# Performance work log

Measured on AMD Instinct MI355X. Metric: run time of the kernel, lower is better.

## Reference

```python
import math
import jax, jax.numpy as jnp
import numpy as np

B, P = 256, 256


def setup_inputs() -> dict:
    key = jax.random.key(0)
    ks = jax.random.split(key, 12)
    sc = 1.0 / math.sqrt(P)
    A = jax.random.normal(ks[0], (B, P, P), jnp.float32) * 0.01
    Theta = jnp.eye(P, dtype=jnp.float32) + 0.5 * (A + A.transpose(0, 2, 1))
    Wb = jax.random.normal(ks[1], (B, P, P), jnp.float32) * 0.01
    W_init = jnp.eye(P, dtype=jnp.float32) + 0.5 * (Wb + Wb.transpose(0, 2, 1))
    return {
        "Theta": Theta,
        "W_init": W_init,
        "Wc": jax.random.normal(ks[2], (P - 1, P - 1), jnp.float32) * sc,
        "bc": jax.random.normal(ks[3], (P - 1,), jnp.float32) * 0.01,
        "A1": jax.random.normal(ks[4], (P, P), jnp.float32) * sc,
        "b1": jax.random.normal(ks[5], (P,), jnp.float32) * 0.01,
        "A2": jax.random.normal(ks[6], (P, P), jnp.float32) * sc,
        "b2": jax.random.normal(ks[7], (P,), jnp.float32) * 0.01,
        "A3": jax.random.normal(ks[8], (1, P), jnp.float32) * sc,
        "b3": jax.random.normal(ks[9], (1,), jnp.float32) * 0.01,
    }


def _spodnet_forward(Theta, W, Wc, bc, A1, b1, A2, b2, A3, b3):
    p = Theta.shape[-1]
    scale = 1.0 / math.sqrt(p)
    # minus_idx[col] = arange(p) with `col` removed  -> [p, p-1]
    minus_idx = jnp.asarray(
        np.array([[j for j in range(p) if j != c] for c in range(p)], dtype=np.int32)
    )

    # ---- pass 1: sequential off-diagonal column update via col_learner ----
    def pass1(Th, col):
        idx = minus_idx[col]                       # [p-1]
        th12 = Th[:, idx, col]                     # [B, p-1]
        th12n = (th12 @ Wc.T + bc) * scale         # Linear(p-1,p-1)/sqrt(p)
        Th = Th.at[:, idx, col].set(th12n)
        Th = Th.at[:, col, idx].set(th12n)
        return Th, None

    Theta, _ = jax.lax.scan(pass1, Theta, jnp.arange(p))

    # ---- pass 2: sequential diagonal + Sherman-Morrison W update ----
    def pass2(carry, col):
        Th, W = carry
        idx = minus_idx[col]
        th12 = Th[:, idx, col]                     # [B, p-1]
        th22 = Th[:, col, col]                     # [B]
        W11 = W[:, idx[:, None], idx[None, :]]     # [B, p-1, p-1]
        w22 = W[:, col, col]                       # [B]
        w12 = W[:, idx, col]                       # [B, p-1]
        # inv(Theta_11) = W_11 - w_12 w_12^T / w_22
        invT11 = W11 - (w12[:, :, None] * w12[:, None, :]) / w22[:, None, None]
        v = jnp.einsum('bij,bj->bi', invT11, th12)          # [B, p-1]
        schur = jnp.einsum('bi,bi->b', th12, v)             # theta_12^T invT11 theta_12
        feats = jnp.concatenate([th22[:, None], th12], -1)  # [B, p]
        h = jax.nn.relu(feats @ A1.T + b1)
        h = jax.nn.relu(h @ A2.T + b2)
        gy = jnp.exp(h @ A3.T + b3)[:, 0]                   # [B], positive
        Th = Th.at[:, col, col].set(gy + schur)
        w22n = 1.0 / gy
        w12n = -w22n[:, None] * v
        W11n = invT11 + gy[:, None, None] * (w12n[:, :, None] * w12n[:, None, :])
        W = W.at[:, idx[:, None], idx[None, :]].set(W11n)
        W = W.at[:, idx, col].set(w12n)
        W = W.at[:, col, idx].set(w12n)
        W = W.at[:, col, col].set(w22n)
        # original detaches every W write -> no grad flows through W history
        W = jax.lax.stop_gradient(W)
        return (Th, W), None

    (Theta, _W), _ = jax.lax.scan(
        pass2, (Theta, jax.lax.stop_gradient(W)), jnp.arange(p)
    )
    return Theta


def reference(Theta, W_init, Wc, bc, A1, b1, A2, b2, A3, b3):
    # K = 1 pass (init_kwargs K=1)
    return _spodnet_forward(Theta, W_init, Wc, bc, A1, b1, A2, b2, A3, b3)
```

## Files before the change

kernel.cpp:

```cpp
#include <hip/hip_runtime.h>
#include <math.h>

#define P    256
#define PM1  255

__global__ void __launch_bounds__(256) k_transpose(
    const float* __restrict__ A1, const float* __restrict__ A2,
    float* __restrict__ A1T, float* __restrict__ A2T) {
  __shared__ float tile[64][65];
  const int bid = blockIdx.x;
  const float* src = (bid < 16) ? A1 : A2;
  float* dst       = (bid < 16) ? A1T : A2T;
  const int tl = bid & 15;
  const int R0 = (tl >> 2) << 6;
  const int C0 = (tl & 3) << 6;
  const int tx = threadIdx.x & 63;
  const int ty = threadIdx.x >> 6;
#pragma unroll
  for (int k = 0; k < 16; k++) {
    const int r = (k << 2) + ty;
    tile[r][tx] = src[(R0 + r) * P + C0 + tx];
  }
  __syncthreads();
#pragma unroll
  for (int k = 0; k < 16; k++) {
    const int c = (k << 2) + ty;
    dst[(C0 + c) * P + R0 + tx] = tile[tx][c];
  }
}

__global__ void __launch_bounds__(512, 2) k_pass1(
    float* __restrict__ Th,
    const float* __restrict__ Wc,
    const float* __restrict__ bc) {
  const int b    = blockIdx.x;
  const int tid  = threadIdx.x;
  const int lane = tid & 63;
  const int wid  = tid >> 6;
  const int wrr  = wid >> 2;
  const int wcb  = wid & 3;
  const int r0   = (wrr << 7) + lane;
  const int r1   = r0 + 64;
  const int cbase = wcb << 6;

  float w0[64], w1[64];
#pragma unroll
  for (int k = 0; k < 64; k++) {
    const int c = cbase + k;
    w0[k] = (r0 < PM1 && c < PM1) ? Wc[r0 * PM1 + c] : 0.f;
    w1[k] = (r1 < PM1 && c < PM1) ? Wc[r1 * PM1 + c] : 0.f;
  }

  __shared__ __align__(16) float t_lds[P];
  __shared__ float ypart[4][P];
  __shared__ float bc_lds[P];
  if (tid < P) bc_lds[tid] = (tid < PM1) ? bc[tid] : 0.f;

  float* __restrict__ ThB = Th + (size_t)b * P * P;
  __syncthreads();

  for (int col = 0; col < P; col++) {
    if (tid < P) {
      float v = 0.f;
      if (tid < PM1) {
        const int i = tid + (tid >= col ? 1 : 0);
        v = ThB[i * P + col];
      }
      t_lds[tid] = v;
    }
    __syncthreads();

    float acc0 = 0.f, acc1 = 0.f;
#pragma unroll
    for (int k4 = 0; k4 < 16; k4++) {
      const float4 t4 = *(const float4*)&t_lds[cbase + (k4 << 2)];
      const float tt[4] = {t4.x, t4.y, t4.z, t4.w};
#pragma unroll
      for (int kk = 0; kk < 4; kk++) {
        acc0 = fmaf(w0[(k4 << 2) + kk], tt[kk], acc0);
        acc1 = fmaf(w1[(k4 << 2) + kk], tt[kk], acc1);
      }
    }
    ypart[wcb][r0] = acc0;
    ypart[wcb][r1] = acc1;
    __syncthreads();

    if (tid < PM1) {
      const float y = (ypart[0][tid] + ypart[1][tid] + ypart[2][tid] +
                       ypart[3][tid] + bc_lds[tid]) * 0.0625f;
      const int iout = tid + (tid >= col ? 1 : 0);
      ThB[iout * P + col] = y;
      ThB[col * P + iout] = y;
    }
    __threadfence_block();
    __syncthreads();
  }
}

__global__ void __launch_bounds__(256, 4) k_mlp(
    const float* __restrict__ Th,
    const float* __restrict__ A1T, const float* __restrict__ b1,
    const float* __restrict__ A2T, const float* __restrict__ b2,
    const float* __restrict__ A3,  const float* __restrict__ b3,
    float* __restrict__ gy) {
  const int m0 = blockIdx.x << 4;
  const int b  = m0 >> 8;
  const int c0 = m0 & (P - 1);
  const int t  = threadIdx.x;

  __shared__ __align__(16) float fbuf[16][260];
  __shared__ __align__(16) float hbuf[16][260];
  __shared__ float A3_lds[P];
  if (t < P) A3_lds[t] = A3[t];

  const float* __restrict__ ThB = Th + (size_t)b * P * P;

  {
    const int cc = t & 15;
    const int dr = t >> 4;
    const int c  = c0 + cc;
#pragma unroll
    for (int ii = 0; ii < 16; ii++) {
      const int i = (ii << 4) + dr;
      const float v = ThB[i * P + c];
      const int pos = (i == c) ? 0 : (i < c ? i + 1 : i);
      fbuf[cc][pos] = v;
    }
  }
  __syncthreads();

  {
    float acc[16];
    const float bv = b1[t];
#pragma unroll
    for (int r = 0; r < 16; r++) acc[r] = bv;
    for (int j4 = 0; j4 < 64; j4++) {
      const int j = j4 << 2;
      const float a0 = A1T[(j + 0) * P + t];
      const float a1 = A1T[(j + 1) * P + t];
      const float a2 = A1T[(j + 2) * P + t];
      const float a3 = A1T[(j + 3) * P + t];
#pragma unroll
      for (int r = 0; r < 16; r++) {
        const float4 f4 = *(const float4*)&fbuf[r][j];
        acc[r] = fmaf(f4.x, a0, acc[r]);
        acc[r] = fmaf(f4.y, a1, acc[r]);
        acc[r] = fmaf(f4.z, a2, acc[r]);
        acc[r] = fmaf(f4.w, a3, acc[r]);
      }
    }
#pragma unroll
    for (int r = 0; r < 16; r++) hbuf[r][t] = fmaxf(acc[r], 0.f);
  }
  __syncthreads();

  {
    float acc[16];
    const float bv = b2[t];
#pragma unroll
    for (int r = 0; r < 16; r++) acc[r] = bv;
    for (int j4 = 0; j4 < 64; j4++) {
      const int j = j4 << 2;
      const float a0 = A2T[(j + 0) * P + t];
      const float a1 = A2T[(j + 1) * P + t];
      const float a2 = A2T[(j + 2) * P + t];
      const float a3 = A2T[(j + 3) * P + t];
#pragma unroll
      for (int r = 0; r < 16; r++) {
        const float4 f4 = *(const float4*)&hbuf[r][j];
        acc[r] = fmaf(f4.x, a0, acc[r]);
        acc[r] = fmaf(f4.y, a1, acc[r]);
        acc[r] = fmaf(f4.z, a2, acc[r]);
        acc[r] = fmaf(f4.w, a3, acc[r]);
      }
    }
    __syncthreads();
#pragma unroll
    for (int r = 0; r < 16; r++) fbuf[r][t] = fmaxf(acc[r], 0.f);
  }
  __syncthreads();

  {
    const int r = t >> 4, sub = t & 15;
    float p = 0.f;
#pragma unroll
    for (int jj = 0; jj < 16; jj++) {
      const int j = (jj << 4) + sub;
      p = fmaf(fbuf[r][j], A3_lds[j], p);
    }
    p += __shfl_xor(p, 1);
    p += __shfl_xor(p, 2);
    p += __shfl_xor(p, 4);
    p += __shfl_xor(p, 8);
    if (sub == 0) gy[m0 + r] = expf(p + b3[0]);
  }
}

__global__ void __launch_bounds__(512, 2) k_pass2(
    float* __restrict__ Th,
    const float* __restrict__ Winit,
    const float* __restrict__ gy) {
  const int b    = blockIdx.x;
  const int tid  = threadIdx.x;
  const int lane = tid & 63;
  const int wid  = tid >> 6;
  const int wrr  = wid >> 2;
  const int wcb  = wid & 3;
  const int r0   = (wrr << 7) + lane;
  const int r1   = r0 + 64;
  const int cbase = wcb << 6;

  float w0[64], w1[64];
  const float* __restrict__ WB = Winit + (size_t)b * P * P;
#pragma unroll
  for (int k4 = 0; k4 < 16; k4++) {
    const float4 v0 = *(const float4*)&WB[r0 * P + cbase + (k4 << 2)];
    const float4 v1 = *(const float4*)&WB[r1 * P + cbase + (k4 << 2)];
    w0[(k4 << 2) + 0] = v0.x; w0[(k4 << 2) + 1] = v0.y;
    w0[(k4 << 2) + 2] = v0.z; w0[(k4 << 2) + 3] = v0.w;
    w1[(k4 << 2) + 0] = v1.x; w1[(k4 << 2) + 1] = v1.y;
    w1[(k4 << 2) + 2] = v1.z; w1[(k4 << 2) + 3] = v1.w;
  }

  float* __restrict__ ThB = Th + (size_t)b * P * P;
  const float* __restrict__ gyB = gy + b * P;

  __shared__ __align__(16) float t_lds[P];
  __shared__ __align__(16) float a_lds[P];
  __shared__ __align__(16) float z_lds[P];
  __shared__ float ypart[4][P];
  __shared__ float red[8];

  float tv = 0.f;
  if (tid < P) tv = ThB[tid * P];
  __syncthreads();

  for (int col = 0; col < P; col++) {
    const int kcol  = col & 63;
    const int wccol = col >> 6;
    const float gyv = gyB[col];

    if (tid < P) t_lds[tid] = (tid == col) ? 0.f : tv;
    if (wcb == wccol) {
      float av0 = 0.f, av1 = 0.f;
#pragma unroll
      for (int k = 0; k < 64; k++) {
        if (k == kcol) { av0 = w0[k]; av1 = w1[k]; }
      }
      a_lds[r0] = av0;
      a_lds[r1] = av1;
    }
    __syncthreads();
    if (tid < P && col < PM1) tv = ThB[tid * P + col + 1];

    const float w22 = a_lds[col];
    if (tid < P) {
      float pp = a_lds[tid] * t_lds[tid];
      pp += __shfl_xor(pp, 1);  pp += __shfl_xor(pp, 2);
      pp += __shfl_xor(pp, 4);  pp += __shfl_xor(pp, 8);
      pp += __shfl_xor(pp, 16); pp += __shfl_xor(pp, 32);
      if (lane == 0) red[wid] = pp;
    }
    __syncthreads();
    const float s = (red[0] + red[1] + red[2] + red[3]) / w22;

    float acc0 = 0.f, acc1 = 0.f;
#pragma unroll
    for (int k4 = 0; k4 < 16; k4++) {
      const float4 t4 = *(const float4*)&t_lds[cbase + (k4 << 2)];
      const float tt[4] = {t4.x, t4.y, t4.z, t4.w};
#pragma unroll
      for (int kk = 0; kk < 4; kk++) {
        acc0 = fmaf(w0[(k4 << 2) + kk], tt[kk], acc0);
        acc1 = fmaf(w1[(k4 << 2) + kk], tt[kk], acc1);
      }
    }
    ypart[wcb][r0] = acc0;
    ypart[wcb][r1] = acc1;
    __syncthreads();

    if (tid < P) {
      const float y = ypart[0][tid] + ypart[1][tid] +
                      ypart[2][tid] + ypart[3][tid];
      const float v = y - a_lds[tid] * s;
      const float z = (tid == col) ? 1.f : -v;
      z_lds[tid] = z;
      float pp = t_lds[tid] * z;
      pp += __shfl_xor(pp, 1);  pp += __shfl_xor(pp, 2);
      pp += __shfl_xor(pp, 4);  pp += __shfl_xor(pp, 8);
      pp += __shfl_xor(pp, 16); pp += __shfl_xor(pp, 32);
      if (lane == 0) red[wid] = pp;
    }
    __syncthreads();
    const float schur = -(red[0] + red[1] + red[2] + red[3]);
    if (tid == 0) ThB[col * P + col] = gyv + schur;

    const float c1 = -1.f / w22;
    const float c2 = 1.f / gyv;
    const float pa0 = c1 * a_lds[r0], pa1 = c1 * a_lds[r1];
    const float pz0 = c2 * z_lds[r0], pz1 = c2 * z_lds[r1];
#pragma unroll
    for (int k4 = 0; k4 < 16; k4++) {
      const float4 a4 = *(const float4*)&a_lds[cbase + (k4 << 2)];
      const float4 z4 = *(const float4*)&z_lds[cbase + (k4 << 2)];
      const float aa[4] = {a4.x, a4.y, a4.z, a4.w};
      const float zz[4] = {z4.x, z4.y, z4.z, z4.w};
#pragma unroll
      for (int kk = 0; kk < 4; kk++) {
        const int k = (k4 << 2) + kk;
        w0[k] = fmaf(pa0, aa[kk], fmaf(pz0, zz[kk], w0[k]));
        w1[k] = fmaf(pa1, aa[kk], fmaf(pz1, zz[kk], w1[k]));
      }
    }
    __syncthreads();
  }
}

extern "C" void kernel_launch(void* const* d_in, const int* in_sizes, int n_in,
                              void* d_out, int out_size, void* d_ws, size_t ws_size,
                              hipStream_t stream) {
  (void)in_sizes; (void)n_in; (void)out_size; (void)ws_size;
  const float* Theta = (const float*)d_in[0];
  const float* Winit = (const float*)d_in[1];
  const float* Wc    = (const float*)d_in[2];
  const float* bc    = (const float*)d_in[3];
  const float* A1    = (const float*)d_in[4];
  const float* b1    = (const float*)d_in[5];
  const float* A2    = (const float*)d_in[6];
  const float* b2    = (const float*)d_in[7];
  const float* A3    = (const float*)d_in[8];
  const float* b3    = (const float*)d_in[9];
  float* out = (float*)d_out;

  float* A1T = (float*)d_ws;
  float* A2T = A1T + P * P;
  float* gy  = A2T + P * P;

  hipMemcpyAsync(out, Theta, (size_t)256 * P * P * sizeof(float),
                 hipMemcpyDeviceToDevice, stream);

  k_transpose<<<32, 256, 0, stream>>>(A1, A2, A1T, A2T);
  k_pass1<<<256, 512, 0, stream>>>(out, Wc, bc);
  k_mlp<<<4096, 256, 0, stream>>>(out, A1T, b1, A2T, b2, A3, b3, gy);
  k_pass2<<<256, 512, 0, stream>>>(out, Winit, gy);
}
```

Baseline: 1.446 ms.

## Double-buffer column vectors and cut barriers in sequential pass kernels

Both sequential column kernels now double-buffer the theta column (and W column in pass2) in LDS and prefetch the next column during the current step. This removes one or two barriers per iteration. Pass1 reads the next column row-wise, which relies on Theta staying symmetric, and forwards the freshly written value. Pass2 drops the register select-scan for the W column in favour of the owning row writing it out, and gets the Schur term from ypart in a spare wave instead of a second block reduction. The cost is more LDS, a dependence on symmetry, and more intricate ordering of reads and writes across iterations.

```diff
diff --git a/kernel.cpp b/kernel.cpp
--- a/kernel.cpp
+++ b/kernel.cpp
@@ -35,8 +35,8 @@
     const float* __restrict__ bc) {
   const int b    = blockIdx.x;
   const int tid  = threadIdx.x;
+  const int wid  = tid >> 6;
   const int lane = tid & 63;
-  const int wid  = tid >> 6;
   const int wrr  = wid >> 2;
   const int wcb  = wid & 3;
   const int r0   = (wrr << 7) + lane;
@@ -51,49 +51,51 @@
     w1[k] = (r1 < PM1 && c < PM1) ? Wc[r1 * PM1 + c] : 0.f;
   }
 
-  __shared__ __align__(16) float t_lds[P];
+  __shared__ __align__(16) float t_buf[2][P];
   __shared__ float ypart[4][P];
   __shared__ float bc_lds[P];
   if (tid < P) bc_lds[tid] = (tid < PM1) ? bc[tid] : 0.f;
 
   float* __restrict__ ThB = Th + (size_t)b * P * P;
-  __syncthreads();
-
+  if (tid < P) t_buf[0][tid] = (tid < PM1) ? ThB[tid + 1] : 0.f;
+
+  int p = 0;
   for (int col = 0; col < P; col++) {
-    if (tid < P) {
-      float v = 0.f;
-      if (tid < PM1) {
-        const int i = tid + (tid >= col ? 1 : 0);
-        v = ThB[i * P + col];
-      }
-      t_lds[tid] = v;
-    }
-    __syncthreads();
-
+    const int pn = p ^ 1;
+    __syncthreads();
     float acc0 = 0.f, acc1 = 0.f;
+    const float4* tb = (const float4*)&t_buf[p][cbase];
 #pragma unroll
     for (int k4 = 0; k4 < 16; k4++) {
-      const float4 t4 = *(const float4*)&t_lds[cbase + (k4 << 2)];
-      const float tt[4] = {t4.x, t4.y, t4.z, t4.w};
-#pragma unroll
-      for (int kk = 0; kk < 4; kk++) {
-        acc0 = fmaf(w0[(k4 << 2) + kk], tt[kk], acc0);
-        acc1 = fmaf(w1[(k4 << 2) + kk], tt[kk], acc1);
-      }
+      const float4 tv = tb[k4];
+      acc0 = fmaf(w0[(k4 << 2) + 0], tv.x, acc0);
+      acc0 = fmaf(w0[(k4 << 2) + 1], tv.y, acc0);
+      acc0 = fmaf(w0[(k4 << 2) + 2], tv.z, acc0);
+      acc0 = fmaf(w0[(k4 << 2) + 3], tv.w, acc0);
+      acc1 = fmaf(w1[(k4 << 2) + 0], tv.x, acc1);
+      acc1 = fmaf(w1[(k4 << 2) + 1], tv.y, acc1);
+      acc1 = fmaf(w1[(k4 << 2) + 2], tv.z, acc1);
+      acc1 = fmaf(w1[(k4 << 2) + 3], tv.w, acc1);
     }
     ypart[wcb][r0] = acc0;
     ypart[wcb][r1] = acc1;
-    __syncthreads();
-
+    float tnext = 0.f;
+    if (col < PM1 && tid < PM1) {
+      const int i = tid + (tid >= col + 1 ? 1 : 0);
+      tnext = ThB[(col + 1) * P + i];
+    }
+    __syncthreads();
     if (tid < PM1) {
       const float y = (ypart[0][tid] + ypart[1][tid] + ypart[2][tid] +
                        ypart[3][tid] + bc_lds[tid]) * 0.0625f;
       const int iout = tid + (tid >= col ? 1 : 0);
       ThB[iout * P + col] = y;
       ThB[col * P + iout] = y;
-    }
-    __threadfence_block();
-    __syncthreads();
+      if (col < PM1) t_buf[pn][tid] = (tid == col) ? y : tnext;
+    } else if (tid == PM1) {
+      t_buf[pn][PM1] = 0.f;
+    }
+    p = pn;
   }
 }
 
@@ -182,17 +184,17 @@
 
   {
     const int r = t >> 4, sub = t & 15;
-    float p = 0.f;
+    float pq = 0.f;
 #pragma unroll
     for (int jj = 0; jj < 16; jj++) {
       const int j = (jj << 4) + sub;
-      p = fmaf(fbuf[r][j], A3_lds[j], p);
-    }
-    p += __shfl_xor(p, 1);
-    p += __shfl_xor(p, 2);
-    p += __shfl_xor(p, 4);
-    p += __shfl_xor(p, 8);
-    if (sub == 0) gy[m0 + r] = expf(p + b3[0]);
+      pq = fmaf(fbuf[r][j], A3_lds[j], pq);
+    }
+    pq += __shfl_xor(pq, 1);
+    pq += __shfl_xor(pq, 2);
+    pq += __shfl_xor(pq, 4);
+    pq += __shfl_xor(pq, 8);
+    if (sub == 0) gy[m0 + r] = expf(pq + b3[0]);
   }
 }
 
@@ -209,6 +211,7 @@
   const int r0   = (wrr << 7) + lane;
   const int r1   = r0 + 64;
   const int cbase = wcb << 6;
+  const int e0   = lane << 2;
 
   float w0[64], w1[64];
   const float* __restrict__ WB = Winit + (size_t)b * P * P;
@@ -225,55 +228,55 @@
   float* __restrict__ ThB = Th + (size_t)b * P * P;
   const float* __restrict__ gyB = gy + b * P;
 
-  __shared__ __align__(16) float t_lds[P];
-  __shared__ __align__(16) float a_lds[P];
+  __shared__ __align__(16) float t_buf[2][P];
+  __shared__ __align__(16) float a_buf[2][P];
   __shared__ __align__(16) float z_lds[P];
   __shared__ float ypart[4][P];
-  __shared__ float red[8];
-
-  float tv = 0.f;
-  if (tid < P) tv = ThB[tid * P];
-  __syncthreads();
-
+
+  if (tid < P) t_buf[0][tid] = (tid == 0) ? 0.f : ThB[tid];
+  if (r0 == 0) {
+    float4* dst = (float4*)&a_buf[0][cbase];
+#pragma unroll
+    for (int k4 = 0; k4 < 16; k4++)
+      dst[k4] = make_float4(w0[(k4 << 2) + 0], w0[(k4 << 2) + 1],
+                            w0[(k4 << 2) + 2], w0[(k4 << 2) + 3]);
+  }
+  float gyv = gyB[0];
+
+  int p = 0;
   for (int col = 0; col < P; col++) {
-    const int kcol  = col & 63;
-    const int wccol = col >> 6;
-    const float gyv = gyB[col];
-
-    if (tid < P) t_lds[tid] = (tid == col) ? 0.f : tv;
-    if (wcb == wccol) {
-      float av0 = 0.f, av1 = 0.f;
-#pragma unroll
-      for (int k = 0; k < 64; k++) {
-        if (k == kcol) { av0 = w0[k]; av1 = w1[k]; }
-      }
-      a_lds[r0] = av0;
-      a_lds[r1] = av1;
-    }
-    __syncthreads();
-    if (tid < P && col < PM1) tv = ThB[tid * P + col + 1];
-
-    const float w22 = a_lds[col];
-    if (tid < P) {
-      float pp = a_lds[tid] * t_lds[tid];
-      pp += __shfl_xor(pp, 1);  pp += __shfl_xor(pp, 2);
-      pp += __shfl_xor(pp, 4);  pp += __shfl_xor(pp, 8);
-      pp += __shfl_xor(pp, 16); pp += __shfl_xor(pp, 32);
-      if (lane == 0) red[wid] = pp;
-    }
-    __syncthreads();
-    const float s = (red[0] + red[1] + red[2] + red[3]) / w22;
+    const int pn = p ^ 1;
+    __syncthreads();
+
+    const float4 a4 = *(const float4*)&a_buf[p][e0];
+    const float4 t4 = *(const float4*)&t_buf[p][e0];
+    float pp = a4.x * t4.x + a4.y * t4.y + a4.z * t4.z + a4.w * t4.w;
+    pp += __shfl_xor(pp, 1);  pp += __shfl_xor(pp, 2);
+    pp += __shfl_xor(pp, 4);  pp += __shfl_xor(pp, 8);
+    pp += __shfl_xor(pp, 16); pp += __shfl_xor(pp, 32);
+    const float at  = pp;
+    const float w22 = a_buf[p][col];
+    const float s   = at / w22;
+
+    float tnext = 0.f, gynext = 0.f;
+    if (col < PM1) {
+      if (tid < P) tnext = ThB[(col + 1) * P + tid];
+      gynext = gyB[col + 1];
+    }
 
     float acc0 = 0.f, acc1 = 0.f;
+    const float4* tb = (const float4*)&t_buf[p][cbase];
 #pragma unroll
     for (int k4 = 0; k4 < 16; k4++) {
-      const float4 t4 = *(const float4*)&t_lds[cbase + (k4 << 2)];
-      const float tt[4] = {t4.x, t4.y, t4.z, t4.w};
-#pragma unroll
-      for (int kk = 0; kk < 4; kk++) {
-        acc0 = fmaf(w0[(k4 << 2) + kk], tt[kk], acc0);
-        acc1 = fmaf(w1[(k4 << 2) + kk], tt[kk], acc1);
-      }
+      const float4 tv = tb[k4];
+      acc0 = fmaf(w0[(k4 << 2) + 0], tv.x, acc0);
+      acc0 = fmaf(w0[(k4 << 2) + 1], tv.y, acc0);
+      acc0 = fmaf(w0[(k4 << 2) + 2], tv.z, acc0);
+      acc0 = fmaf(w0[(k4 << 2) + 3], tv.w, acc0);
+      acc1 = fmaf(w1[(k4 << 2) + 0], tv.x, acc1);
+      acc1 = fmaf(w1[(k4 << 2) + 1], tv.y, acc1);
+      acc1 = fmaf(w1[(k4 << 2) + 2], tv.z, acc1);
+      acc1 = fmaf(w1[(k4 << 2) + 3], tv.w, acc1);
     }
     ypart[wcb][r0] = acc0;
     ypart[wcb][r1] = acc1;
@@ -282,37 +285,62 @@
     if (tid < P) {
       const float y = ypart[0][tid] + ypart[1][tid] +
                       ypart[2][tid] + ypart[3][tid];
-      const float v = y - a_lds[tid] * s;
-      const float z = (tid == col) ? 1.f : -v;
-      z_lds[tid] = z;
-      float pp = t_lds[tid] * z;
-      pp += __shfl_xor(pp, 1);  pp += __shfl_xor(pp, 2);
-      pp += __shfl_xor(pp, 4);  pp += __shfl_xor(pp, 8);
-      pp += __shfl_xor(pp, 16); pp += __shfl_xor(pp, 32);
-      if (lane == 0) red[wid] = pp;
-    }
-    __syncthreads();
-    const float schur = -(red[0] + red[1] + red[2] + red[3]);
-    if (tid == 0) ThB[col * P + col] = gyv + schur;
+      const float v = y - s * a_buf[p][tid];
+      z_lds[tid] = (tid == col) ? 1.f : -v;
+      if (col < PM1) t_buf[pn][tid] = (tid == col + 1) ? 0.f : tnext;
+    } else if (wid == 4) {
+      const float4 tt = *(const float4*)&t_buf[p][e0];
+      const float4 q0 = *(const float4*)&ypart[0][e0];
+      const float4 q1 = *(const float4*)&ypart[1][e0];
+      const float4 q2 = *(const float4*)&ypart[2][e0];
+      const float4 q3 = *(const float4*)&ypart[3][e0];
+      float sp = tt.x * (q0.x + q1.x + q2.x + q3.x)
+               + tt.y * (q0.y + q1.y + q2.y + q3.y)
+               + tt.z * (q0.z + q1.z + q2.z + q3.z)
+               + tt.w * (q0.w + q1.w + q2.w + q3.w);
+      sp += __shfl_xor(sp, 1);  sp += __shfl_xor(sp, 2);
+      sp += __shfl_xor(sp, 4);  sp += __shfl_xor(sp, 8);
+      sp += __shfl_xor(sp, 16); sp += __shfl_xor(sp, 32);
+      if (lane == 0) ThB[col * P + col] = gyv + (sp - s * at);
+    }
+    __syncthreads();
 
     const float c1 = -1.f / w22;
     const float c2 = 1.f / gyv;
-    const float pa0 = c1 * a_lds[r0], pa1 = c1 * a_lds[r1];
-    const float pz0 = c2 * z_lds[r0], pz1 = c2 * z_lds[r1];
+    const float pa0 = c1 * a_buf[p][r0], pa1 = c1 * a_buf[p][r1];
+    const float pz0 = c2 * z_lds[r0],    pz1 = c2 * z_lds[r1];
+    const float4* ab = (const float4*)&a_buf[p][cbase];
+    const float4* zb = (const float4*)&z_lds[cbase];
 #pragma unroll
     for (int k4 = 0; k4 < 16; k4++) {
-      const float4 a4 = *(const float4*)&a_lds[cbase + (k4 << 2)];
-      const float4 z4 = *(const float4*)&z_lds[cbase + (k4 << 2)];
-      const float aa[4] = {a4.x, a4.y, a4.z, a4.w};
-      const float zz[4] = {z4.x, z4.y, z4.z, z4.w};
-#pragma unroll
-      for (int kk = 0; kk < 4; kk++) {
-        const int k = (k4 << 2) + kk;
-        w0[k] = fmaf(pa0, aa[kk], fmaf(pz0, zz[kk], w0[k]));
-        w1[k] = fmaf(pa1, aa[kk], fmaf(pz1, zz[kk], w1[k]));
-      }
-    }
-    __syncthreads();
+      const float4 av = ab[k4];
+      const float4 zv = zb[k4];
+      w0[(k4 << 2) + 0] = fmaf(pa0, av.x, fmaf(pz0, zv.x, w0[(k4 << 2) + 0]));
+      w0[(k4 << 2) + 1] = fmaf(pa0, av.y, fmaf(pz0, zv.y, w0[(k4 << 2) + 1]));
+      w0[(k4 << 2) + 2] = fmaf(pa0, av.z, fmaf(pz0, zv.z, w0[(k4 << 2) + 2]));
+      w0[(k4 << 2) + 3] = fmaf(pa0, av.w, fmaf(pz0, zv.w, w0[(k4 << 2) + 3]));
+      w1[(k4 << 2) + 0] = fmaf(pa1, av.x, fmaf(pz1, zv.x, w1[(k4 << 2) + 0]));
+      w1[(k4 << 2) + 1] = fmaf(pa1, av.y, fmaf(pz1, zv.y, w1[(k4 << 2) + 1]));
+      w1[(k4 << 2) + 2] = fmaf(pa1, av.z, fmaf(pz1, zv.z, w1[(k4 << 2) + 2]));
+      w1[(k4 << 2) + 3] = fmaf(pa1, av.w, fmaf(pz1, zv.w, w1[(k4 << 2) + 3]));
+    }
+
+    if (r0 == col + 1) {
+      float4* dst = (float4*)&a_buf[pn][cbase];
+#pragma unroll
+      for (int k4 = 0; k4 < 16; k4++)
+        dst[k4] = make_float4(w0[(k4 << 2) + 0], w0[(k4 << 2) + 1],
+                              w0[(k4 << 2) + 2], w0[(k4 << 2) + 3]);
+    } else if (r1 == col + 1) {
+      float4* dst = (float4*)&a_buf[pn][cbase];
+#pragma unroll
+      for (int k4 = 0; k4 < 16; k4++)
+        dst[k4] = make_float4(w1[(k4 << 2) + 0], w1[(k4 << 2) + 1],
+                              w1[(k4 << 2) + 2], w1[(k4 << 2) + 3]);
+    }
+
+    gyv = gynext;
+    p = pn;
   }
 }
 
@@ -334,13 +362,13 @@
 
   float* A1T = (float*)d_ws;
   float* A2T = A1T + P * P;
-  float* gy  = A2T + P * P;
+  float* gyb = A2T + P * P;
 
   hipMemcpyAsync(out, Theta, (size_t)256 * P * P * sizeof(float),
                  hipMemcpyDeviceToDevice, stream);
 
   k_transpose<<<32, 256, 0, stream>>>(A1, A2, A1T, A2T);
   k_pass1<<<256, 512, 0, stream>>>(out, Wc, bc);
-  k_mlp<<<4096, 256, 0, stream>>>(out, A1T, b1, A2T, b2, A3, b3, gy);
-  k_pass2<<<256, 512, 0, stream>>>(out, Winit, gy);
-}
+  k_mlp<<<4096, 256, 0, stream>>>(out, A1T, b1, A2T, b2, A3, b3, gyb);
+  k_pass2<<<256, 512, 0, stream>>>(out, Winit, gyb);
+}
```

Result: faster. 1.409 ms (-2.5%).
